# Kernel optimization log

Measured on AMD Instinct MI355X. Metric: run time of the kernel, lower is better.

Reference implementation:

```python
import jax, jax.numpy as jnp
import numpy as np

VOCAB, EMB, HID, SEQ = 50257, 512, 512, 4096


def setup_inputs() -> dict:
    key = jax.random.key(0)
    k1, k2, k3, k4, k5, k6 = jax.random.split(key, 6)
    s = 1.0 / np.sqrt(HID)
    return {
        "tokens": jax.random.randint(k1, (SEQ,), 0, VOCAB),
        "emb": jax.random.normal(k2, (VOCAB, EMB), jnp.float32) * 0.02,
        "W_ih": jax.random.normal(k3, (4 * HID, EMB), jnp.float32) * s,
        "W_hh": jax.random.normal(k4, (4 * HID, HID), jnp.float32) * s,
        "b_ih": jax.random.normal(k5, (4 * HID,), jnp.float32) * s,
        "b_hh": jax.random.normal(k6, (4 * HID,), jnp.float32) * s,
    }


def reference(tokens, emb, W_ih, W_hh, b_ih, b_hh):
    # gather all embeddings once: [S, E]
    xs = emb[tokens]
    # precompute input-to-gate projections for all steps: [S, 4H]
    gx = xs @ W_ih.T + b_ih + b_hh
    H = W_hh.shape[1]

    def step(carry, gx_t):
        h, c = carry
        gates = gx_t + h @ W_hh.T  # [4H]
        i, f, g, o = jnp.split(gates, 4)
        i = jax.nn.sigmoid(i)
        f = jax.nn.sigmoid(f)
        g = jnp.tanh(g)
        o = jax.nn.sigmoid(o)
        c = f * c + i * g
        h = o * jnp.tanh(c)
        return (h, c), None

    h0 = jnp.zeros((H,), xs.dtype)
    c0 = jnp.zeros((H,), xs.dtype)
    (h, c), _ = jax.lax.scan(step, (h0, c0), gx)
    return (h, c)
```

## Files before the change

### kernel.cpp

```cpp
#include <hip/hip_runtime.h>
#include <hip/hip_bf16.h>

#define SEQ   4096
#define HID   512
#define GDIM  2048
#define NSCAN 64
#define GRID_SCAN 512
#define SPIN_CAP 65536

#define GX_BYTES   (33554432L)
#define INIT_WORDS 4106

typedef unsigned uint;
typedef uint  v4u __attribute__((ext_vector_type(4)));
typedef uint  v2u __attribute__((ext_vector_type(2)));
typedef _Float16 half2v __attribute__((ext_vector_type(2)));

static __device__ __forceinline__ half2v pack_f16(float a, float b) {
    return __builtin_bit_cast(half2v, __builtin_amdgcn_cvt_pkrtz(a, b));
}

#if __has_builtin(__builtin_amdgcn_fdot2)
#define FDOT2(a,b,c) __builtin_amdgcn_fdot2((a),(b),(c),false)
#else
static __device__ __forceinline__ float FDOT2(half2v a, half2v b, float c) {
    return c + (float)a.x * (float)b.x + (float)a.y * (float)b.y;
}
#endif

__global__ __launch_bounds__(256) void gemm_gx(
    const int*   __restrict__ tokens,
    const float* __restrict__ emb,
    const float* __restrict__ W_ih,
    const float* __restrict__ b_ih,
    const float* __restrict__ b_hh,
    float*       __restrict__ gx,
    int*         __restrict__ initzone)
{
    __shared__ float As[64][33];
    __shared__ float Bs[64][33];
    __shared__ int   tok_s[64];

    const int tid = threadIdx.x;
    const int j0  = blockIdx.x * 64;
    const int t0  = blockIdx.y * 64;

    if (blockIdx.x == 0 && blockIdx.y == 0) {
        for (int i = tid; i < INIT_WORDS; i += 256) initzone[i] = 0;
    }
    if (tid < 64) tok_s[tid] = tokens[t0 + tid];
    __syncthreads();

    const int i  = tid >> 2;
    const int ko = (tid & 3) * 8;
    const int ty = tid >> 4;
    const int tx = tid & 15;

    const long arow = (long)tok_s[i] * HID;
    const long brow = (long)(j0 + i) * HID;

    float acc[4][4] = {};

    for (int k0 = 0; k0 < HID; k0 += 32) {
        float4 a0 = *(const float4*)&emb[arow + k0 + ko];
        float4 a1 = *(const float4*)&emb[arow + k0 + ko + 4];
        float4 b0 = *(const float4*)&W_ih[brow + k0 + ko];
        float4 b1 = *(const float4*)&W_ih[brow + k0 + ko + 4];
        As[i][ko+0]=a0.x; As[i][ko+1]=a0.y; As[i][ko+2]=a0.z; As[i][ko+3]=a0.w;
        As[i][ko+4]=a1.x; As[i][ko+5]=a1.y; As[i][ko+6]=a1.z; As[i][ko+7]=a1.w;
        Bs[i][ko+0]=b0.x; Bs[i][ko+1]=b0.y; Bs[i][ko+2]=b0.z; Bs[i][ko+3]=b0.w;
        Bs[i][ko+4]=b1.x; Bs[i][ko+5]=b1.y; Bs[i][ko+6]=b1.z; Bs[i][ko+7]=b1.w;
        __syncthreads();

        #pragma unroll
        for (int kk = 0; kk < 32; ++kk) {
            float av0 = As[ty*4+0][kk], av1 = As[ty*4+1][kk];
            float av2 = As[ty*4+2][kk], av3 = As[ty*4+3][kk];
            float bv0 = Bs[tx*4+0][kk], bv1 = Bs[tx*4+1][kk];
            float bv2 = Bs[tx*4+2][kk], bv3 = Bs[tx*4+3][kk];
            acc[0][0] += av0*bv0; acc[0][1] += av0*bv1; acc[0][2] += av0*bv2; acc[0][3] += av0*bv3;
            acc[1][0] += av1*bv0; acc[1][1] += av1*bv1; acc[1][2] += av1*bv2; acc[1][3] += av1*bv3;
            acc[2][0] += av2*bv0; acc[2][1] += av2*bv1; acc[2][2] += av2*bv2; acc[2][3] += av2*bv3;
            acc[3][0] += av3*bv0; acc[3][1] += av3*bv1; acc[3][2] += av3*bv2; acc[3][3] += av3*bv3;
        }
        __syncthreads();
    }

    #pragma unroll
    for (int m = 0; m < 4; ++m) {
        const long t = t0 + ty*4 + m;
        #pragma unroll
        for (int n = 0; n < 4; ++n) {
            const int j = j0 + tx*4 + n;
            gx[t*GDIM + j] = acc[m][n] + b_ih[j] + b_hh[j];
        }
    }
}

__global__ __launch_bounds__(256, 2) void lstm_scan(
    const float* __restrict__ gx,
    const float* __restrict__ W_hh,
    unsigned long long* hp,
    unsigned long long* hp2,
    uint*  elect,
    float* out)
{
    __shared__ uint s_part[2];
    __shared__ uint hs16[2][8 * 36];

    const int tid = threadIdx.x;

    uint xcd;
    asm volatile("s_getreg_b32 %0, hwreg(HW_REG_XCC_ID)" : "=s"(xcd));
    xcd &= 7u;
    if (tid == 0) {
        uint* xcnt    = elect;
        uint* winlock = elect + 8;
        uint* winner  = elect + 9;
        uint slot = __hip_atomic_fetch_add(&xcnt[xcd], 1u,
                        __ATOMIC_RELAXED, __HIP_MEMORY_SCOPE_AGENT);
        if (slot == NSCAN - 1) {
            if (__hip_atomic_fetch_add(winlock, 1u,
                    __ATOMIC_ACQ_REL, __HIP_MEMORY_SCOPE_AGENT) == 0)
                __hip_atomic_store(winner, xcd + 1u,
                    __ATOMIC_RELEASE, __HIP_MEMORY_SCOPE_AGENT);
        }
        uint wn;
        while ((wn = __hip_atomic_load(winner,
                    __ATOMIC_ACQUIRE, __HIP_MEMORY_SCOPE_AGENT)) == 0)
            __builtin_amdgcn_s_sleep(2);
        s_part[0] = (wn - 1u == xcd && slot < NSCAN) ? 1u : 0u;
        s_part[1] = slot;
    }
    __syncthreads();
    if (!s_part[0]) return;
    const int w = (int)s_part[1];

    const int wv = tid >> 6;
    const int l  = tid & 63;
    const int r  = l >> 3;
    const int c  = l & 7;
    const int g  = r >> 1;
    const int uu = r & 1;
    const int unit  = w * 8 + wv * 2 + uu;
    const int grow  = g * 512 + unit;
    const int selu  = (l >= 32) ? 1 : 0;
    const int punit = w * 8 + wv * 2 + selu;

    half2v wreg[32];
    {
        const float* wsrc = W_hh + (long)grow * HID + c * 64;
        #pragma unroll
        for (int j = 0; j < 32; ++j) {
            float2 wp = *(const float2*)&wsrc[2 * j];
            wreg[j] = pack_f16(wp.x, wp.y);
        }
    }

    float cstate = 0.0f;
    float gxcur = (c == 0) ? gx[grow] : 0.0f;

    const int cc  = tid >> 5;
    const int pos = tid & 31;
    bool slow = true;

    for (int t = 0; t < SEQ; ++t) {
        const int p = t & 1;

        v4u pv;
        bool ok = false;
        if (!slow) {
            const unsigned long long* src = hp + (long)p * HID + 2 * tid;
            for (int spin = 0; spin < SPIN_CAP; ++spin) {
                asm volatile("global_load_dwordx4 %0, %1, off sc0\n\t"
                             "s_waitcnt vmcnt(0)"
                             : "=v"(pv) : "v"(src) : "memory");
                if (pv.y == (uint)t && pv.w == (uint)t) { ok = true; break; }
            }
            if (!ok) slow = true;
        }
        if (slow && !ok) {
            const unsigned long long* s2 = hp2 + (long)p * HID + 2 * tid;
            unsigned long long v0, v1;
            do {
                v0 = __hip_atomic_load(s2, __ATOMIC_RELAXED, __HIP_MEMORY_SCOPE_AGENT);
            } while ((uint)(v0 >> 32) != (uint)t);
            do {
                v1 = __hip_atomic_load(s2 + 1, __ATOMIC_RELAXED, __HIP_MEMORY_SCOPE_AGENT);
            } while ((uint)(v1 >> 32) != (uint)t);
            pv.x = (uint)v0; pv.y = (uint)(v0 >> 32);
            pv.z = (uint)v1; pv.w = (uint)(v1 >> 32);
        }

        half2v h2 = pack_f16(__uint_as_float(pv.x), __uint_as_float(pv.z));
        hs16[p][cc * 36 + pos] = *(uint*)&h2;

        float gxn = 0.0f;
        if (c == 0 && t + 1 < SEQ) gxn = gx[(long)(t + 1) * GDIM + grow];

        __syncthreads();

        uint hh[32];
        #pragma unroll
        for (int j = 0; j < 32; j += 4)
            *(v4u*)&hh[j] = *(const v4u*)&hs16[p][c * 36 + j];

        float acc = 0.0f;
        #pragma unroll
        for (int j = 0; j < 32; ++j)
            acc = FDOT2(wreg[j], *(half2v*)&hh[j], acc);

        acc += __shfl_xor(acc, 1, 64);
        acc += __shfl_xor(acc, 2, 64);
        acc += __shfl_xor(acc, 4, 64);

        const float accg = acc + gxcur;
        gxcur = gxn;

        const float gi = __shfl(accg, 8 * (0 + selu), 64);
        const float gf = __shfl(accg, 8 * (2 + selu), 64);
        const float gc = __shfl(accg, 8 * (4 + selu), 64);
        const float go = __shfl(accg, 8 * (6 + selu), 64);

        const float ig = 1.0f / (1.0f + __expf(-gi));
        const float fg = 1.0f / (1.0f + __expf(-gf));
        const float gg = 2.0f / (1.0f + __expf(-2.0f * gc)) - 1.0f;
        const float og = 1.0f / (1.0f + __expf(-go));
        cstate = fg * cstate + ig * gg;
        const float tc = 2.0f / (1.0f + __expf(-2.0f * cstate)) - 1.0f;
        const float hnew = og * tc;

        if ((l & 31) == 0) {
            const long off = (long)((t + 1) & 1) * HID + punit;
            v2u pub;
            pub.x = __float_as_uint(hnew);
            pub.y = (uint)(t + 1);
            asm volatile("global_store_dwordx2 %0, %1, off sc0"
                         :: "v"(hp + off), "v"(pub) : "memory");
            const unsigned long long mv =
                ((unsigned long long)(uint)(t + 1) << 32) | __float_as_uint(hnew);
            __hip_atomic_store(hp2 + off, mv,
                               __ATOMIC_RELAXED, __HIP_MEMORY_SCOPE_AGENT);
            if (t == SEQ - 1) {
                out[punit]       = hnew;
                out[HID + punit] = cstate;
            }
        }
    }
}

extern "C" void kernel_launch(void* const* d_in, const int* in_sizes, int n_in,
                              void* d_out, int out_size, void* d_ws, size_t ws_size,
                              hipStream_t stream)
{
    const int*   tokens = (const int*)  d_in[0];
    const float* emb    = (const float*)d_in[1];
    const float* W_ih   = (const float*)d_in[2];
    const float* W_hh   = (const float*)d_in[3];
    const float* b_ih   = (const float*)d_in[4];
    const float* b_hh   = (const float*)d_in[5];
    float* out = (float*)d_out;

    char* ws = (char*)d_ws;
    float*              gx    = (float*)ws;
    unsigned long long* hp    = (unsigned long long*)(ws + GX_BYTES);
    unsigned long long* hp2   = (unsigned long long*)(ws + GX_BYTES + 8192);
    uint*               elect = (uint*)(ws + GX_BYTES + 16384);
    int*                initz = (int*)(ws + GX_BYTES);

    gemm_gx<<<dim3(GDIM / 64, SEQ / 64), 256, 0, stream>>>(
        tokens, emb, W_ih, b_ih, b_hh, gx, initz);

    lstm_scan<<<dim3(GRID_SCAN), 256, 0, stream>>>(gx, W_hh, hp, hp2, elect, out);
}
```

Baseline: 8.589 ms.

## Add dedicated producer wave for h polling and gx prefetch in LSTM scan

Adds a fifth wavefront per block that spins on the published hidden state, writes it into shared memory, and prefetches the gx values into LDS, so the four compute waves only wait at a barrier and then compute. Published h values are now packed as two fp16 values per 64-bit slot with a step tag, which halves the number of slots each block must poll, and the dead dual-path publish to hp is removed. The dot product is split across two accumulators to shorten the dependency chain. This adds a producer/consumer barrier handoff with a 320-thread block, and the whole step still serialises on cross-block latency.

```diff
diff --git a/kernel.cpp b/kernel.cpp
--- a/kernel.cpp
+++ b/kernel.cpp
@@ -6,14 +6,12 @@
 #define GDIM  2048
 #define NSCAN 64
 #define GRID_SCAN 512
-#define SPIN_CAP 65536
 
 #define GX_BYTES   (33554432L)
 #define INIT_WORDS 4106
 
 typedef unsigned uint;
 typedef uint  v4u __attribute__((ext_vector_type(4)));
-typedef uint  v2u __attribute__((ext_vector_type(2)));
 typedef _Float16 half2v __attribute__((ext_vector_type(2)));
 
 static __device__ __forceinline__ half2v pack_f16(float a, float b) {
@@ -97,7 +95,7 @@
     }
 }
 
-__global__ __launch_bounds__(256, 2) void lstm_scan(
+__global__ __launch_bounds__(320, 2) void lstm_scan(
     const float* __restrict__ gx,
     const float* __restrict__ W_hh,
     unsigned long long* hp,
@@ -105,8 +103,10 @@
     uint*  elect,
     float* out)
 {
-    __shared__ uint s_part[2];
-    __shared__ uint hs16[2][8 * 36];
+    (void)hp;
+    __shared__ uint  s_part[2];
+    __shared__ uint  hs16[2][8 * 36];
+    __shared__ float gxs[2][32];
 
     const int tid = threadIdx.x;
 
@@ -138,14 +138,71 @@
 
     const int wv = tid >> 6;
     const int l  = tid & 63;
+
+    if (wv == 4) {
+        const bool gl    = (l < 32);
+        const long gxcol = (long)(w * 8) + (long)(l >> 3) * 512 + (l & 7);
+        const int  hoff  = (l >> 3) * 36 + 4 * (l & 7);
+        const unsigned long long* s0 = hp2 + 4 * l;
+        const unsigned long long* s1 = hp2 + 256 + 4 * l;
+
+        float gxA = 0.f, gxB = 0.f;
+        if (gl) gxA = gx[gxcol];
+
+        for (int t = 0; t < SEQ; t += 2) {
+            if (gl) gxB = gx[(long)(t + 1) * GDIM + gxcol];
+            unsigned long long v0, v1, v2, v3;
+            {
+                const uint e = (uint)t;
+                for (;;) {
+                    v0 = __hip_atomic_load(s0 + 0, __ATOMIC_RELAXED, __HIP_MEMORY_SCOPE_AGENT);
+                    v1 = __hip_atomic_load(s0 + 1, __ATOMIC_RELAXED, __HIP_MEMORY_SCOPE_AGENT);
+                    v2 = __hip_atomic_load(s0 + 2, __ATOMIC_RELAXED, __HIP_MEMORY_SCOPE_AGENT);
+                    v3 = __hip_atomic_load(s0 + 3, __ATOMIC_RELAXED, __HIP_MEMORY_SCOPE_AGENT);
+                    if (((uint)(v0 >> 32) == e) & ((uint)(v1 >> 32) == e) &
+                        ((uint)(v2 >> 32) == e) & ((uint)(v3 >> 32) == e)) break;
+                }
+            }
+            {
+                v4u hv; hv.x = (uint)v0; hv.y = (uint)v1; hv.z = (uint)v2; hv.w = (uint)v3;
+                *(v4u*)&hs16[0][hoff] = hv;
+                if (gl) gxs[0][l] = gxA;
+            }
+            __syncthreads();
+
+            if (gl && t + 2 < SEQ) gxA = gx[(long)(t + 2) * GDIM + gxcol];
+            {
+                const uint e = (uint)(t + 1);
+                for (;;) {
+                    v0 = __hip_atomic_load(s1 + 0, __ATOMIC_RELAXED, __HIP_MEMORY_SCOPE_AGENT);
+                    v1 = __hip_atomic_load(s1 + 1, __ATOMIC_RELAXED, __HIP_MEMORY_SCOPE_AGENT);
+                    v2 = __hip_atomic_load(s1 + 2, __ATOMIC_RELAXED, __HIP_MEMORY_SCOPE_AGENT);
+                    v3 = __hip_atomic_load(s1 + 3, __ATOMIC_RELAXED, __HIP_MEMORY_SCOPE_AGENT);
+                    if (((uint)(v0 >> 32) == e) & ((uint)(v1 >> 32) == e) &
+                        ((uint)(v2 >> 32) == e) & ((uint)(v3 >> 32) == e)) break;
+                }
+            }
+            {
+                v4u hv; hv.x = (uint)v0; hv.y = (uint)v1; hv.z = (uint)v2; hv.w = (uint)v3;
+                *(v4u*)&hs16[1][hoff] = hv;
+                if (gl) gxs[1][l] = gxB;
+            }
+            __syncthreads();
+        }
+        return;
+    }
+
     const int r  = l >> 3;
     const int c  = l & 7;
     const int g  = r >> 1;
     const int uu = r & 1;
-    const int unit  = w * 8 + wv * 2 + uu;
-    const int grow  = g * 512 + unit;
-    const int selu  = (l >= 32) ? 1 : 0;
-    const int punit = w * 8 + wv * 2 + selu;
+    const int unit   = w * 8 + wv * 2 + uu;
+    const int grow   = g * 512 + unit;
+    const int selu   = (l >= 32) ? 1 : 0;
+    const int punit  = w * 8 + wv * 2 + selu;
+    const int pubidx = w * 4 + wv;
+    const int gxi    = g * 8 + wv * 2 + uu;
+    const int coff   = c * 36;
 
     half2v wreg[32];
     {
@@ -158,64 +215,32 @@
     }
 
     float cstate = 0.0f;
-    float gxcur = (c == 0) ? gx[grow] : 0.0f;
-
-    const int cc  = tid >> 5;
-    const int pos = tid & 31;
-    bool slow = true;
 
     for (int t = 0; t < SEQ; ++t) {
         const int p = t & 1;
-
-        v4u pv;
-        bool ok = false;
-        if (!slow) {
-            const unsigned long long* src = hp + (long)p * HID + 2 * tid;
-            for (int spin = 0; spin < SPIN_CAP; ++spin) {
-                asm volatile("global_load_dwordx4 %0, %1, off sc0\n\t"
-                             "s_waitcnt vmcnt(0)"
-                             : "=v"(pv) : "v"(src) : "memory");
-                if (pv.y == (uint)t && pv.w == (uint)t) { ok = true; break; }
-            }
-            if (!ok) slow = true;
-        }
-        if (slow && !ok) {
-            const unsigned long long* s2 = hp2 + (long)p * HID + 2 * tid;
-            unsigned long long v0, v1;
-            do {
-                v0 = __hip_atomic_load(s2, __ATOMIC_RELAXED, __HIP_MEMORY_SCOPE_AGENT);
-            } while ((uint)(v0 >> 32) != (uint)t);
-            do {
-                v1 = __hip_atomic_load(s2 + 1, __ATOMIC_RELAXED, __HIP_MEMORY_SCOPE_AGENT);
-            } while ((uint)(v1 >> 32) != (uint)t);
-            pv.x = (uint)v0; pv.y = (uint)(v0 >> 32);
-            pv.z = (uint)v1; pv.w = (uint)(v1 >> 32);
-        }
-
-        half2v h2 = pack_f16(__uint_as_float(pv.x), __uint_as_float(pv.z));
-        hs16[p][cc * 36 + pos] = *(uint*)&h2;
-
-        float gxn = 0.0f;
-        if (c == 0 && t + 1 < SEQ) gxn = gx[(long)(t + 1) * GDIM + grow];
-
         __syncthreads();
 
+        float gxcur = 0.f;
+        if (c == 0) gxcur = gxs[p][gxi];
+
         uint hh[32];
         #pragma unroll
         for (int j = 0; j < 32; j += 4)
-            *(v4u*)&hh[j] = *(const v4u*)&hs16[p][c * 36 + j];
-
-        float acc = 0.0f;
-        #pragma unroll
-        for (int j = 0; j < 32; ++j)
-            acc = FDOT2(wreg[j], *(half2v*)&hh[j], acc);
+            *(v4u*)&hh[j] = *(const v4u*)&hs16[p][coff + j];
+
+        float a0 = 0.f, a1 = 0.f;
+        #pragma unroll
+        for (int j = 0; j < 32; j += 2) {
+            a0 = FDOT2(wreg[j],     *(half2v*)&hh[j],     a0);
+            a1 = FDOT2(wreg[j + 1], *(half2v*)&hh[j + 1], a1);
+        }
+        float acc = a0 + a1;
 
         acc += __shfl_xor(acc, 1, 64);
         acc += __shfl_xor(acc, 2, 64);
         acc += __shfl_xor(acc, 4, 64);
 
         const float accg = acc + gxcur;
-        gxcur = gxn;
 
         const float gi = __shfl(accg, 8 * (0 + selu), 64);
         const float gf = __shfl(accg, 8 * (2 + selu), 64);
@@ -230,21 +255,18 @@
         const float tc = 2.0f / (1.0f + __expf(-2.0f * cstate)) - 1.0f;
         const float hnew = og * tc;
 
-        if ((l & 31) == 0) {
-            const long off = (long)((t + 1) & 1) * HID + punit;
-            v2u pub;
-            pub.x = __float_as_uint(hnew);
-            pub.y = (uint)(t + 1);
-            asm volatile("global_store_dwordx2 %0, %1, off sc0"
-                         :: "v"(hp + off), "v"(pub) : "memory");
+        const float hB = __shfl(hnew, 32, 64);
+        if (l == 0) {
+            half2v ph = pack_f16(hnew, hB);
             const unsigned long long mv =
-                ((unsigned long long)(uint)(t + 1) << 32) | __float_as_uint(hnew);
-            __hip_atomic_store(hp2 + off, mv,
+                ((unsigned long long)(uint)(t + 1) << 32) |
+                (unsigned long long)(*(uint*)&ph);
+            __hip_atomic_store(hp2 + (long)((t + 1) & 1) * 256 + pubidx, mv,
                                __ATOMIC_RELAXED, __HIP_MEMORY_SCOPE_AGENT);
-            if (t == SEQ - 1) {
-                out[punit]       = hnew;
-                out[HID + punit] = cstate;
-            }
+        }
+        if (t == SEQ - 1 && (l & 31) == 0) {
+            out[punit]       = hnew;
+            out[HID + punit] = cstate;
         }
     }
 }
@@ -271,5 +293,5 @@
     gemm_gx<<<dim3(GDIM / 64, SEQ / 64), 256, 0, stream>>>(
         tokens, emb, W_ih, b_ih, b_hh, gx, initz);
 
-    lstm_scan<<<dim3(GRID_SCAN), 256, 0, stream>>>(gx, W_hh, hp, hp2, elect, out);
-}
+    lstm_scan<<<dim3(GRID_SCAN), 320, 0, stream>>>(gx, W_hh, hp, hp2, elect, out);
+}
```

Result: slower. 18.76 ms (+118.5%).

## Publish packed fp16 hidden pairs with one flag word per wave

Applied to the files above, without the earlier changes.

Each wave now packs its two hidden outputs into one fp16x2 word, tagged with the step number, and publishes it in a single 64-bit atomic store. This replaces two fp32 stores to two separate buffers. Consumers poll one 64-bit word per thread instead of two, which halves the cross-block polling traffic and removes the unused fast spin path. The dot product also uses two accumulators to shorten the dependency chain. Rounding to fp16 at publish time matches what the old code did when packing into shared memory.

```diff
diff --git a/kernel.cpp b/kernel.cpp
--- a/kernel.cpp
+++ b/kernel.cpp
@@ -6,14 +6,12 @@
 #define GDIM  2048
 #define NSCAN 64
 #define GRID_SCAN 512
-#define SPIN_CAP 65536
 
 #define GX_BYTES   (33554432L)
 #define INIT_WORDS 4106
 
 typedef unsigned uint;
 typedef uint  v4u __attribute__((ext_vector_type(4)));
-typedef uint  v2u __attribute__((ext_vector_type(2)));
 typedef _Float16 half2v __attribute__((ext_vector_type(2)));
 
 static __device__ __forceinline__ half2v pack_f16(float a, float b) {
@@ -105,6 +103,7 @@
     uint*  elect,
     float* out)
 {
+    (void)hp;
     __shared__ uint s_part[2];
     __shared__ uint hs16[2][8 * 36];
 
@@ -146,6 +145,9 @@
     const int grow  = g * 512 + unit;
     const int selu  = (l >= 32) ? 1 : 0;
     const int punit = w * 8 + wv * 2 + selu;
+    const int pubslot = w * 4 + wv;
+    const int cc  = tid >> 5;
+    const int pos = tid & 31;
 
     half2v wreg[32];
     {
@@ -160,44 +162,20 @@
     float cstate = 0.0f;
     float gxcur = (c == 0) ? gx[grow] : 0.0f;
 
-    const int cc  = tid >> 5;
-    const int pos = tid & 31;
-    bool slow = true;
-
     for (int t = 0; t < SEQ; ++t) {
         const int p = t & 1;
 
-        v4u pv;
-        bool ok = false;
-        if (!slow) {
-            const unsigned long long* src = hp + (long)p * HID + 2 * tid;
-            for (int spin = 0; spin < SPIN_CAP; ++spin) {
-                asm volatile("global_load_dwordx4 %0, %1, off sc0\n\t"
-                             "s_waitcnt vmcnt(0)"
-                             : "=v"(pv) : "v"(src) : "memory");
-                if (pv.y == (uint)t && pv.w == (uint)t) { ok = true; break; }
-            }
-            if (!ok) slow = true;
-        }
-        if (slow && !ok) {
-            const unsigned long long* s2 = hp2 + (long)p * HID + 2 * tid;
-            unsigned long long v0, v1;
-            do {
-                v0 = __hip_atomic_load(s2, __ATOMIC_RELAXED, __HIP_MEMORY_SCOPE_AGENT);
-            } while ((uint)(v0 >> 32) != (uint)t);
-            do {
-                v1 = __hip_atomic_load(s2 + 1, __ATOMIC_RELAXED, __HIP_MEMORY_SCOPE_AGENT);
-            } while ((uint)(v1 >> 32) != (uint)t);
-            pv.x = (uint)v0; pv.y = (uint)(v0 >> 32);
-            pv.z = (uint)v1; pv.w = (uint)(v1 >> 32);
-        }
-
-        half2v h2 = pack_f16(__uint_as_float(pv.x), __uint_as_float(pv.z));
-        hs16[p][cc * 36 + pos] = *(uint*)&h2;
-
         float gxn = 0.0f;
         if (c == 0 && t + 1 < SEQ) gxn = gx[(long)(t + 1) * GDIM + grow];
 
+        unsigned long long v;
+        const unsigned long long* src = hp2 + (long)p * 256 + tid;
+        do {
+            v = __hip_atomic_load(src, __ATOMIC_RELAXED, __HIP_MEMORY_SCOPE_AGENT);
+        } while ((uint)(v >> 32) != (uint)t);
+
+        hs16[p][cc * 36 + pos] = (uint)v;
+
         __syncthreads();
 
         uint hh[32];
@@ -205,10 +183,13 @@
         for (int j = 0; j < 32; j += 4)
             *(v4u*)&hh[j] = *(const v4u*)&hs16[p][c * 36 + j];
 
-        float acc = 0.0f;
-        #pragma unroll
-        for (int j = 0; j < 32; ++j)
-            acc = FDOT2(wreg[j], *(half2v*)&hh[j], acc);
+        float a0 = 0.0f, a1 = 0.0f;
+        #pragma unroll
+        for (int j = 0; j < 32; j += 2) {
+            a0 = FDOT2(wreg[j],     *(half2v*)&hh[j],     a0);
+            a1 = FDOT2(wreg[j + 1], *(half2v*)&hh[j + 1], a1);
+        }
+        float acc = a0 + a1;
 
         acc += __shfl_xor(acc, 1, 64);
         acc += __shfl_xor(acc, 2, 64);
@@ -230,21 +211,18 @@
         const float tc = 2.0f / (1.0f + __expf(-2.0f * cstate)) - 1.0f;
         const float hnew = og * tc;
 
-        if ((l & 31) == 0) {
-            const long off = (long)((t + 1) & 1) * HID + punit;
-            v2u pub;
-            pub.x = __float_as_uint(hnew);
-            pub.y = (uint)(t + 1);
-            asm volatile("global_store_dwordx2 %0, %1, off sc0"
-                         :: "v"(hp + off), "v"(pub) : "memory");
+        const float hB = __shfl(hnew, 32, 64);
+        if (l == 0) {
+            half2v ph = pack_f16(hnew, hB);
             const unsigned long long mv =
-                ((unsigned long long)(uint)(t + 1) << 32) | __float_as_uint(hnew);
-            __hip_atomic_store(hp2 + off, mv,
+                ((unsigned long long)(uint)(t + 1) << 32) |
+                (unsigned long long)(*(uint*)&ph);
+            __hip_atomic_store(hp2 + (long)((t + 1) & 1) * 256 + pubslot, mv,
                                __ATOMIC_RELAXED, __HIP_MEMORY_SCOPE_AGENT);
-            if (t == SEQ - 1) {
-                out[punit]       = hnew;
-                out[HID + punit] = cstate;
-            }
+        }
+        if (t == SEQ - 1 && (l & 31) == 0) {
+            out[punit]       = hnew;
+            out[HID + punit] = cstate;
         }
     }
 }
```

Measured after the change: 13.38 ms. +55.8%, slower.
